# Optimization experiments

Hardware: AMD Instinct MI355X
Metric: run time of the kernel (lower is better)

The kernel has to match this reference:

```python
import jax, jax.numpy as jnp
import numpy as np

S, B, E, H, V, L = 128, 64, 512, 1024, 10000, 2


def setup_inputs() -> dict:
    key = jax.random.key(0)
    ks = jax.random.split(key, 10)
    s = 0.02  # weight scale ~ uniform(-k,k) magnitude
    return {
        "inputs": jax.random.randint(ks[0], (S, B), 0, V),
        "hidden": jnp.zeros((L, B, H), jnp.float32),
        "emb": jax.random.normal(ks[1], (V, E), jnp.float32) * 0.1,
        "Wx0": jax.random.normal(ks[2], (3, H, E), jnp.float32) * s,
        "Uh0": jax.random.normal(ks[3], (3, H, H), jnp.float32) * s,
        "b0": jax.random.normal(ks[4], (3, H), jnp.float32) * s,
        "Wx1": jax.random.normal(ks[5], (3, H, H), jnp.float32) * s,
        "Uh1": jax.random.normal(ks[6], (3, H, H), jnp.float32) * s,
        "b1": jax.random.normal(ks[7], (3, H), jnp.float32) * s,
        "Wd": jax.random.normal(ks[8], (V, H), jnp.float32) * 0.1,
        "bd": jnp.zeros((V,), jnp.float32),
    }


def _gru_cell(xp, h, U, b):
    # xp: (3,B,H) precomputed input projections in [r,z,h] order
    r = jax.nn.sigmoid(xp[0] + h @ U[0].T + b[0])
    z = jax.nn.sigmoid(xp[1] + h @ U[1].T + b[1])
    h_tilde = jnp.tanh(xp[2] + (r * h) @ U[2].T + b[2])
    return (1.0 - z) * h + z * h_tilde


def reference(inputs, hidden, emb, Wx0, Uh0, b0, Wx1, Uh1, b1, Wd, bd):
    x_embs = emb[inputs]                                   # [S,B,E]
    # precompute layer-0 input projections across all timesteps
    xa0 = jnp.einsum("sbe,goe->sgbo", x_embs, Wx0)        # [S,3,B,H]

    def step(carry, xa0_t):
        h0, h1 = carry
        h0n = _gru_cell(xa0_t, h0, Uh0, b0)
        xp1 = jnp.einsum("bk,gok->gbo", h0n, Wx1)          # [3,B,H]
        h1n = _gru_cell(xp1, h1, Uh1, b1)
        return (h0n, h1n), h1n

    (h0f, h1f), hs1 = jax.lax.scan(step, (hidden[0], hidden[1]), xa0)
    logits = jnp.einsum("sbh,vh->sbv", hs1, Wd) + bd       # [S,B,V]
    return logits, jnp.stack([h0f, h1f])
```

## Files before the change

### kernel.cpp

```cpp
#include <hip/hip_runtime.h>
#include <hip/hip_bf16.h>

#define SLEN 128
#define BAT 64
#define EDIM 512
#define HDIM 1024
#define VOC 10000
#define VPAD 10112
#define NWG_REC 192
#define TPB_REC 512

typedef short v8s __attribute__((ext_vector_type(8)));
typedef float v4f __attribute__((ext_vector_type(4)));
typedef unsigned short u16;

__device__ __forceinline__ u16 f2bf(float f) {
  unsigned u = __float_as_uint(f);
  u += 0x7fffu + ((u >> 16) & 1u);
  return (u16)(u >> 16);
}
__device__ __forceinline__ float bf2f(u16 b) {
  return __uint_as_float(((unsigned)b) << 16);
}
__device__ __forceinline__ float sigm(float x) { return 1.f / (1.f + __expf(-x)); }
__device__ __forceinline__ float tanh_f(float x) { return 1.f - 2.f / (1.f + __expf(2.f * x)); }

__device__ __forceinline__ void st_f32(float* p, float v) {
  __hip_atomic_store(p, v, __ATOMIC_RELAXED, __HIP_MEMORY_SCOPE_AGENT);
}
__device__ __forceinline__ float ld_f32(const float* p) {
  return __hip_atomic_load(p, __ATOMIC_RELAXED, __HIP_MEMORY_SCOPE_AGENT);
}
__device__ __forceinline__ float ld_bf16(const unsigned* base, int elem) {
  unsigned pr = __hip_atomic_load(base + (elem >> 1), __ATOMIC_RELAXED, __HIP_MEMORY_SCOPE_AGENT);
  return bf2f((u16)((elem & 1) ? (pr >> 16) : (pr & 0xffffu)));
}
__device__ __forceinline__ void st_bf16_pair(unsigned* base, int elem, u16 val, int l) {
  unsigned p = (unsigned)__shfl_xor((int)val, 1);
  if ((l & 1) == 0)
    __hip_atomic_store(base + (elem >> 1), (unsigned)val | (p << 16),
                       __ATOMIC_RELAXED, __HIP_MEMORY_SCOPE_AGENT);
}

__device__ __forceinline__ void gbar_full(int* bar, int ph, int wg, int t) {
  asm volatile("s_waitcnt vmcnt(0) lgkmcnt(0)" ::: "memory");
  __syncthreads();
  if (t == 0)
    __hip_atomic_store(&bar[wg], ph, __ATOMIC_RELAXED, __HIP_MEMORY_SCOPE_AGENT);
  if (t < 64) {
    for (;;) {
      int v0 = __hip_atomic_load(&bar[t],       __ATOMIC_RELAXED, __HIP_MEMORY_SCOPE_AGENT);
      int v1 = __hip_atomic_load(&bar[64 + t],  __ATOMIC_RELAXED, __HIP_MEMORY_SCOPE_AGENT);
      int v2 = __hip_atomic_load(&bar[128 + t], __ATOMIC_RELAXED, __HIP_MEMORY_SCOPE_AGENT);
      if (__all((v0 >= ph) & (v1 >= ph) & (v2 >= ph))) break;
      __builtin_amdgcn_s_sleep(1);
    }
  }
  __syncthreads();
}

__device__ __forceinline__ void gbar_inv(int* bar, int ph, int wg, int t,
                                         int xcc, bool lead) {
  asm volatile("s_waitcnt vmcnt(0) lgkmcnt(0)" ::: "memory");
  __syncthreads();
  if (t == 0)
    __hip_atomic_store(&bar[wg], ph, __ATOMIC_RELAXED, __HIP_MEMORY_SCOPE_AGENT);
  if (lead) {
    if (t < 64) {
      for (;;) {
        int v0 = __hip_atomic_load(&bar[t],       __ATOMIC_RELAXED, __HIP_MEMORY_SCOPE_AGENT);
        int v1 = __hip_atomic_load(&bar[64 + t],  __ATOMIC_RELAXED, __HIP_MEMORY_SCOPE_AGENT);
        int v2 = __hip_atomic_load(&bar[128 + t], __ATOMIC_RELAXED, __HIP_MEMORY_SCOPE_AGENT);
        if (__all((v0 >= ph) & (v1 >= ph) & (v2 >= ph))) break;
        __builtin_amdgcn_s_sleep(1);
      }
      if (t == 0) {
        asm volatile("buffer_inv sc1" ::: "memory");
        asm volatile("s_waitcnt vmcnt(0)" ::: "memory");
        __hip_atomic_store(&bar[256 + xcc], ph, __ATOMIC_RELAXED, __HIP_MEMORY_SCOPE_AGENT);
      }
    }
  } else {
    if (t < 64) {
      while (__hip_atomic_load(&bar[256 + xcc], __ATOMIC_RELAXED, __HIP_MEMORY_SCOPE_AGENT) < ph)
        __builtin_amdgcn_s_sleep(1);
    }
  }
  if (t < 64) {
    asm volatile("buffer_inv" ::: "memory");
    asm volatile("s_waitcnt vmcnt(0)" ::: "memory");
  }
  __syncthreads();
}

__device__ __forceinline__ v4f gemm_staged(const char* Asrc, char* stage,
                                           const char* bb, int swz,
                                           int t, int rg, int lr, int lk2) {
  const char* gp = Asrc + (t >> 3) * 2048 + (t & 7) * 16;
  char* wp = stage + (t >> 3) * 128 + (((t & 7) * 16) ^ (((t >> 3) & 7) << 4));
  const char* rp = stage + (rg * 16 + lr) * 128;
  v4f acc{0.f, 0.f, 0.f, 0.f};
  v8s sreg[3];
  asm volatile("global_load_dwordx4 %0, %1, off" : "=v"(sreg[0]) : "v"(gp));
  asm volatile("global_load_dwordx4 %0, %1, off offset:128" : "=v"(sreg[1]) : "v"(gp));
  asm volatile("global_load_dwordx4 %0, %1, off offset:256" : "=v"(sreg[2]) : "v"(gp));
  asm volatile("s_waitcnt vmcnt(2)" ::: "memory");
  __builtin_amdgcn_sched_barrier(0);
  *(v8s*)wp = sreg[0];
  __syncthreads();
#pragma unroll
  for (int c = 0; c < 16; ++c) {
    if (c < 13)
      asm volatile("global_load_dwordx4 %0, %1, off offset:%2"
                   : "=v"(sreg[c % 3]) : "v"(gp), "i"((c + 3) * 128));
    if (c < 15) {
      if (c < 13)       asm volatile("s_waitcnt vmcnt(2)" ::: "memory");
      else if (c == 13) asm volatile("s_waitcnt vmcnt(1)" ::: "memory");
      else              asm volatile("s_waitcnt vmcnt(0)" ::: "memory");
      __builtin_amdgcn_sched_barrier(0);
      *(v8s*)(wp + ((c + 1) & 1) * 8192) = sreg[(c + 1) % 3];
    }
    const char* buf = rp + (c & 1) * 8192;
#pragma unroll
    for (int ls = 0; ls < 2; ++ls) {
      v8s a = *(const v8s*)(buf + ((ls * 64 + lk2) ^ swz));
      v8s b = *(const v8s*)(bb + (((c * 2 + ls) * 64 + lk2) ^ swz));
      acc = __builtin_amdgcn_mfma_f32_16x16x32_bf16(a, b, acc, 0, 0, 0);
    }
    __syncthreads();
  }
  return acc;
}

__global__ void __launch_bounds__(TPB_REC, 2) k_recur(
    const u16* __restrict__ Uh0b, const u16* __restrict__ Wx1b, const u16* __restrict__ Uh1b,
    const float* __restrict__ b0, const float* __restrict__ b1,
    const u16* __restrict__ xa0,
    float* __restrict__ h0f, u16* __restrict__ h0b,
    float* __restrict__ h1f, u16* __restrict__ h1b,
    u16* __restrict__ a2, float* __restrict__ z0,
    u16* __restrict__ a5, float* __restrict__ z1,
    u16* __restrict__ xp1,
    u16* __restrict__ hs1,
    float* __restrict__ outh,
    int* __restrict__ bar) {
  extern __shared__ char smem[];
  const int wg = blockIdx.x;
  const int t = threadIdx.x;
  const int w = t >> 6;
  const int l = t & 63;
  const int lr = l & 15;
  const int lk2 = (l >> 4) * 16;
  const int rg = w >> 1, cg = w & 1;
  const int rbase = rg * 16 + ((l >> 4) << 2);
  const int swz = (lr & 7) << 4;
  char* stage = smem + 131072;

  unsigned* a2u  = (unsigned*)a2;
  unsigned* a5u  = (unsigned*)a5;
  unsigned* h0bu = (unsigned*)h0b;
  unsigned* h1bu = (unsigned*)h1b;
  unsigned* xpu  = (unsigned*)xp1;
  unsigned* hs1u = (unsigned*)hs1;

  {
    const u16* w1src; int w1row0;
    if (wg < 64)       { w1src = Uh0b; w1row0 = wg * 32; }
    else if (wg < 160) { w1src = Wx1b; w1row0 = (wg - 64) * 32; }
    else               { w1src = Uh1b; w1row0 = 2048 + (wg - 160) * 32; }
    for (int i = t; i < 4096; i += TPB_REC) {
      int c = i >> 7, j = i & 127;
      v8s v = *(const v8s*)(w1src + (size_t)(w1row0 + c) * HDIM + j * 8);
      *(v8s*)(smem + c * 2048 + ((j * 16) ^ ((c & 7) << 4))) = v;
    }
    if (wg < 96) {
      const u16* w2src; int w2row0;
      if (wg < 32) { w2src = Uh0b; w2row0 = 2048 + wg * 32; }
      else         { w2src = Uh1b; w2row0 = (wg - 32) * 32; }
      for (int i = t; i < 4096; i += TPB_REC) {
        int c = i >> 7, j = i & 127;
        v8s v = *(const v8s*)(w2src + (size_t)(w2row0 + c) * HDIM + j * 8);
        *(v8s*)(smem + 65536 + c * 2048 + ((j * 16) ^ ((c & 7) << 4))) = v;
      }
    }
    __syncthreads();
  }

  int xcc;
  asm volatile("s_getreg_b32 %0, hwreg(HW_REG_XCC_ID)" : "=s"(xcc));
  xcc &= 7;
  if (t == 0)
    (void)__hip_atomic_fetch_min(&bar[320 + xcc], wg, __ATOMIC_RELAXED, __HIP_MEMORY_SCOPE_AGENT);
  gbar_full(bar, 1, wg, t);
  const bool lead =
      (__hip_atomic_load(&bar[320 + xcc], __ATOMIC_RELAXED, __HIP_MEMORY_SCOPE_AGENT) == wg);

  const char* bb1 = smem + (cg * 16 + lr) * 2048;
  const char* bb2 = smem + 65536 + (cg * 16 + lr) * 2048;

  for (int T = 0; T <= SLEN + 1; ++T) {
    if (wg < 64) {
      if (T < SLEN) {
        const int cglob = wg * 32 + cg * 16 + lr;
        const int g = cglob >> 10;
        const int o = cglob & 1023;
        const float bias = b0[g * HDIM + o];
        float xv[4], hv[4];
#pragma unroll
        for (int r = 0; r < 4; ++r) {
          int b = rbase + r;
          xv[r] = bf2f(xa0[((T * 3 + g) * BAT + b) * HDIM + o]);
          if (g == 0) hv[r] = ld_f32(&h0f[b * HDIM + o]);
        }
        v4f acc = gemm_staged((const char*)h0b, stage, bb1, swz, t, rg, lr, lk2);
#pragma unroll
        for (int r = 0; r < 4; ++r) {
          int b = rbase + r;
          float s = sigm(acc[r] + xv[r] + bias);
          if (g == 0) st_bf16_pair(a2u, b * HDIM + o, f2bf(s * hv[r]), l);
          else        st_f32(&z0[b * HDIM + o], s);
        }
      }
    } else if (wg < 160) {
      if (T >= 1 && T <= SLEN) {
        const int n = (wg - 64) * 32 + cg * 16 + lr;
        v4f acc = gemm_staged((const char*)h0b, stage, bb1, swz, t, rg, lr, lk2);
        unsigned* xp = xpu + ((((T - 1) & 1) * (BAT * 3 * HDIM)) >> 1);
#pragma unroll
        for (int r = 0; r < 4; ++r)
          st_bf16_pair(xp, (rbase + r) * 3072 + n, f2bf(acc[r]), l);
      }
    } else {
      if (T >= 2) {
        const int t5 = T - 2;
        const int o = (wg - 160) * 32 + cg * 16 + lr;
        const unsigned* xp = xpu + (((t5 & 1) * (BAT * 3 * HDIM)) >> 1);
        const float bias = b1[2 * HDIM + o];
        float pv[4], zv[4], hv[4];
#pragma unroll
        for (int r = 0; r < 4; ++r) {
          int b = rbase + r;
          pv[r] = ld_bf16(xp, b * 3072 + 2048 + o);
          zv[r] = ld_f32(&z1[b * HDIM + o]);
          hv[r] = ld_f32(&h1f[b * HDIM + o]);
        }
        v4f acc = gemm_staged((const char*)a5, stage, bb1, swz, t, rg, lr, lk2);
#pragma unroll
        for (int r = 0; r < 4; ++r) {
          int b = rbase + r;
          float ht = tanh_f(pv[r] + acc[r] + bias);
          float hn = (1.f - zv[r]) * hv[r] + zv[r] * ht;
          u16 hb = f2bf(hn);
          st_f32(&h1f[b * HDIM + o], hn);
          st_bf16_pair(h1bu, b * HDIM + o, hb, l);
          st_bf16_pair(hs1u, (int)(((size_t)t5 * BAT + b) * HDIM + o), hb, l);
          if (t5 == SLEN - 1) st_f32(&outh[(size_t)BAT * HDIM + b * HDIM + o], hn);
        }
      }
    }
    gbar_inv(bar, 2 * T + 2, wg, t, xcc, lead);
    if (wg < 32) {
      if (T < SLEN) {
        const int o = wg * 32 + cg * 16 + lr;
        const float bias = b0[2 * HDIM + o];
        float xv[4], zv[4], hv[4];
#pragma unroll
        for (int r = 0; r < 4; ++r) {
          int b = rbase + r;
          xv[r] = bf2f(xa0[((T * 3 + 2) * BAT + b) * HDIM + o]);
          zv[r] = ld_f32(&z0[b * HDIM + o]);
          hv[r] = ld_f32(&h0f[b * HDIM + o]);
        }
        v4f acc = gemm_staged((const char*)a2, stage, bb2, swz, t, rg, lr, lk2);
#pragma unroll
        for (int r = 0; r < 4; ++r) {
          int b = rbase + r;
          float ht = tanh_f(xv[r] + acc[r] + bias);
          float hn = (1.f - zv[r]) * hv[r] + zv[r] * ht;
          st_f32(&h0f[b * HDIM + o], hn);
          st_bf16_pair(h0bu, b * HDIM + o, f2bf(hn), l);
          if (T == SLEN - 1) st_f32(&outh[b * HDIM + o], hn);
        }
      }
    } else if (wg < 96) {
      if (T >= 1 && T <= SLEN) {
        const int t4 = T - 1;
        const int cglob = (wg - 32) * 32 + cg * 16 + lr;
        const int g = cglob >> 10;
        const int o = cglob & 1023;
        const unsigned* xp = xpu + (((t4 & 1) * (BAT * 3 * HDIM)) >> 1);
        const float bias = b1[g * HDIM + o];
        float pv[4], hv[4];
#pragma unroll
        for (int r = 0; r < 4; ++r) {
          int b = rbase + r;
          pv[r] = ld_bf16(xp, b * 3072 + g * HDIM + o);
          if (g == 0) hv[r] = ld_f32(&h1f[b * HDIM + o]);
        }
        v4f acc = gemm_staged((const char*)h1b, stage, bb2, swz, t, rg, lr, lk2);
#pragma unroll
        for (int r = 0; r < 4; ++r) {
          int b = rbase + r;
          float s = sigm(acc[r] + pv[r] + bias);
          if (g == 0) st_bf16_pair(a5u, b * HDIM + o, f2bf(s * hv[r]), l);
          else        st_f32(&z1[b * HDIM + o], s);
        }
      }
    }
    gbar_inv(bar, 2 * T + 3, wg, t, xcc, lead);
  }
}

template <int MODE>
__global__ void __launch_bounds__(256) k_gemm(
    const u16* __restrict__ A, const u16* __restrict__ Bw,
    const int* __restrict__ gidx, const float* __restrict__ bias,
    void* __restrict__ Out) {
  constexpr int K = MODE ? 1024 : 512;
  constexpr int NB_N = MODE ? (VPAD / 128) : (3072 / 128);

  __shared__ u16 sA[128 * 64];
  __shared__ u16 sB[128 * 64];

  const int nwg = gridDim.x;
  const int cpx = nwg >> 3;
  const int bid = blockIdx.x;
  const int swz = (bid & 7) * cpx + (bid >> 3);
  const int bm = swz / NB_N, bn = swz % NB_N;
  const int m0 = bm * 128, n0 = bn * 128;

  const int t = threadIdx.x;
  const int w = t >> 6, l = t & 63;
  const int lr = l & 15, lk = (l >> 4) * 8;
  const int wm = (w >> 1) * 64, wn = (w & 1) * 64;
  const int kc = (t & 7) * 8;

  int arowg[4];
#pragma unroll
  for (int i = 0; i < 4; ++i) {
    int row = m0 + i * 32 + (t >> 3);
    arowg[i] = (MODE == 0) ? gidx[row] : row;
  }
  int brow[4];
#pragma unroll
  for (int i = 0; i < 4; ++i) brow[i] = n0 + i * 32 + (t >> 3);

  v4f acc[4][4];
#pragma unroll
  for (int mi = 0; mi < 4; ++mi)
#pragma unroll
    for (int ni = 0; ni < 4; ++ni) acc[mi][ni] = v4f{0.f, 0.f, 0.f, 0.f};

  for (int k0 = 0; k0 < K; k0 += 64) {
    __syncthreads();
#pragma unroll
    for (int i = 0; i < 4; ++i) {
      const u16* src = A + (size_t)arowg[i] * K + k0 + kc;
      __builtin_amdgcn_global_load_lds((const __attribute__((address_space(1))) void*)src,
                                       (__attribute__((address_space(3))) void*)(sA + i * 2048 + w * 512),
                                       16, 0, 0);
    }
#pragma unroll
    for (int i = 0; i < 4; ++i) {
      const u16* src = Bw + (size_t)brow[i] * K + k0 + kc;
      __builtin_amdgcn_global_load_lds((const __attribute__((address_space(1))) void*)src,
                                       (__attribute__((address_space(3))) void*)(sB + i * 2048 + w * 512),
                                       16, 0, 0);
    }
    asm volatile("s_waitcnt vmcnt(0)" ::: "memory");
    __syncthreads();
#pragma unroll
    for (int ks = 0; ks < 2; ++ks) {
      v8s af[4], bfr[4];
#pragma unroll
      for (int mi = 0; mi < 4; ++mi) af[mi] = *(const v8s*)&sA[(wm + mi * 16 + lr) * 64 + ks * 32 + lk];
#pragma unroll
      for (int ni = 0; ni < 4; ++ni) bfr[ni] = *(const v8s*)&sB[(wn + ni * 16 + lr) * 64 + ks * 32 + lk];
#pragma unroll
      for (int mi = 0; mi < 4; ++mi)
#pragma unroll
        for (int ni = 0; ni < 4; ++ni)
          acc[mi][ni] = __builtin_amdgcn_mfma_f32_16x16x32_bf16(af[mi], bfr[ni], acc[mi][ni], 0, 0, 0);
    }
  }

#pragma unroll
  for (int mi = 0; mi < 4; ++mi)
#pragma unroll
    for (int ni = 0; ni < 4; ++ni)
#pragma unroll
      for (int r = 0; r < 4; ++r) {
        int grow = m0 + wm + mi * 16 + ((l >> 4) << 2) + r;
        int gcol = n0 + wn + ni * 16 + lr;
        float v = acc[mi][ni][r];
        if (MODE == 0) {
          int s = grow >> 6, b = grow & 63;
          int g = gcol >> 10, o = gcol & 1023;
          ((u16*)Out)[(((size_t)s * 3 + g) * BAT + b) * HDIM + o] = f2bf(v);
        } else {
          if (gcol < VOC) ((float*)Out)[(size_t)grow * VOC + gcol] = v + bias[gcol];
        }
      }
}

__global__ void k_cvt(const float* __restrict__ src, u16* __restrict__ dst, int n, int nsrc) {
  int i = (blockIdx.x * 256 + threadIdx.x) * 4;
  if (i >= n) return;
#pragma unroll
  for (int j = 0; j < 4; ++j) {
    int idx = i + j;
    if (idx < n) dst[idx] = (idx < nsrc) ? f2bf(src[idx]) : (u16)0;
  }
}

__global__ void k_init(const float* __restrict__ hidden,
                       float* h0f, u16* h0b, float* h1f, u16* h1b, int* bar) {
  int i = blockIdx.x * 256 + threadIdx.x;
  if (i < BAT * HDIM) {
    float v0 = hidden[i];
    float v1 = hidden[BAT * HDIM + i];
    h0f[i] = v0; h0b[i] = f2bf(v0);
    h1f[i] = v1; h1b[i] = f2bf(v1);
  }
  if (i < 512) bar[i] = (i >= 320 && i < 328) ? 0x7fffffff : 0;
}

extern "C" void kernel_launch(void* const* d_in, const int* in_sizes, int n_in,
                              void* d_out, int out_size, void* d_ws, size_t ws_size,
                              hipStream_t stream) {
  const int*   inp = (const int*)d_in[0];
  const float* hid = (const float*)d_in[1];
  const float* emb = (const float*)d_in[2];
  const float* Wx0 = (const float*)d_in[3];
  const float* Uh0 = (const float*)d_in[4];
  const float* b0  = (const float*)d_in[5];
  const float* Wx1 = (const float*)d_in[6];
  const float* Uh1 = (const float*)d_in[7];
  const float* b1  = (const float*)d_in[8];
  const float* Wd  = (const float*)d_in[9];
  const float* bd  = (const float*)d_in[10];

  char* ws = (char*)d_ws;
  size_t off = 0;
  auto alloc = [&](size_t bytes) {
    void* p = ws + off;
    off = (off + bytes + 255) & ~(size_t)255;
    return p;
  };
  u16* emb_b = (u16*)alloc(sizeof(u16) * (size_t)VOC * EDIM);
  u16* Wx0_b = (u16*)alloc(sizeof(u16) * 3 * HDIM * EDIM);
  u16* Uh0_b = (u16*)alloc(sizeof(u16) * 3 * HDIM * HDIM);
  u16* Wx1_b = (u16*)alloc(sizeof(u16) * 3 * HDIM * HDIM);
  u16* Uh1_b = (u16*)alloc(sizeof(u16) * 3 * HDIM * HDIM);
  u16* Wd_b  = (u16*)alloc(sizeof(u16) * (size_t)VPAD * HDIM);
  u16* xa0_b = (u16*)alloc(sizeof(u16) * (size_t)SLEN * 3 * BAT * HDIM);
  u16* hs1_b = (u16*)alloc(sizeof(u16) * (size_t)SLEN * BAT * HDIM);
  u16* xp1   = (u16*)alloc(sizeof(u16) * 2 * BAT * 3 * HDIM);
  float* h0f = (float*)alloc(sizeof(float) * BAT * HDIM);
  float* h1f = (float*)alloc(sizeof(float) * BAT * HDIM);
  u16* h0b   = (u16*)alloc(sizeof(u16) * BAT * HDIM);
  u16* h1b   = (u16*)alloc(sizeof(u16) * BAT * HDIM);
  u16* a2    = (u16*)alloc(sizeof(u16) * BAT * HDIM);
  u16* a5    = (u16*)alloc(sizeof(u16) * BAT * HDIM);
  float* z0  = (float*)alloc(sizeof(float) * BAT * HDIM);
  float* z1  = (float*)alloc(sizeof(float) * BAT * HDIM);
  int* bar   = (int*)alloc(sizeof(int) * 512);

  float* logits = (float*)d_out;
  float* outh = logits + (size_t)SLEN * BAT * VOC;

  auto cvt = [&](const float* s, u16* d, int n, int nsrc) {
    k_cvt<<<dim3((n / 4 + 255) / 256), dim3(256), 0, stream>>>(s, d, n, nsrc);
  };
  cvt(emb, emb_b, VOC * EDIM, VOC * EDIM);
  cvt(Wx0, Wx0_b, 3 * HDIM * EDIM, 3 * HDIM * EDIM);
  cvt(Uh0, Uh0_b, 3 * HDIM * HDIM, 3 * HDIM * HDIM);
  cvt(Wx1, Wx1_b, 3 * HDIM * HDIM, 3 * HDIM * HDIM);
  cvt(Uh1, Uh1_b, 3 * HDIM * HDIM, 3 * HDIM * HDIM);
  cvt(Wd, Wd_b, VPAD * HDIM, VOC * HDIM);
  k_init<<<dim3(256), dim3(256), 0, stream>>>(hid, h0f, h0b, h1f, h1b, bar);

  k_gemm<0><<<dim3(64 * 24), dim3(256), 0, stream>>>(emb_b, Wx0_b, inp, (const float*)nullptr, (void*)xa0_b);

  (void)hipFuncSetAttribute(reinterpret_cast<const void*>(k_recur),
                            hipFuncAttributeMaxDynamicSharedMemorySize, 147456);
  k_recur<<<dim3(NWG_REC), dim3(TPB_REC), 147456, stream>>>(
      Uh0_b, Wx1_b, Uh1_b, b0, b1, xa0_b,
      h0f, h0b, h1f, h1b, a2, z0, a5, z1, xp1, hs1_b, outh, bar);

  k_gemm<1><<<dim3(64 * 79), dim3(256), 0, stream>>>(hs1_b, Wd_b, (const int*)nullptr, bd, d_out);
}
```

Before: 2.476 ms.

## Load recurrent GEMM activations directly from global into registers, dropping LDS staging

Replaces the LDS-staged A-operand path in the recurrent kernel's per-step GEMM with direct global loads into registers, keeping eight loads in flight. It accumulates into two alternating MFMA accumulators. This removes the per-chunk __syncthreads and LDS write/read round-trips, and shrinks dynamic shared memory by 16 KB. Each wave now fetches its own A rows from global/L2, so the two column-group waves load the same data twice, and more registers are used.

```diff
diff --git a/kernel.cpp b/kernel.cpp
--- a/kernel.cpp
+++ b/kernel.cpp
@@ -93,43 +93,26 @@
   __syncthreads();
 }
 
-__device__ __forceinline__ v4f gemm_staged(const char* Asrc, char* stage,
-                                           const char* bb, int swz,
-                                           int t, int rg, int lr, int lk2) {
-  const char* gp = Asrc + (t >> 3) * 2048 + (t & 7) * 16;
-  char* wp = stage + (t >> 3) * 128 + (((t & 7) * 16) ^ (((t >> 3) & 7) << 4));
-  const char* rp = stage + (rg * 16 + lr) * 128;
-  v4f acc{0.f, 0.f, 0.f, 0.f};
-  v8s sreg[3];
-  asm volatile("global_load_dwordx4 %0, %1, off" : "=v"(sreg[0]) : "v"(gp));
-  asm volatile("global_load_dwordx4 %0, %1, off offset:128" : "=v"(sreg[1]) : "v"(gp));
-  asm volatile("global_load_dwordx4 %0, %1, off offset:256" : "=v"(sreg[2]) : "v"(gp));
-  asm volatile("s_waitcnt vmcnt(2)" ::: "memory");
-  __builtin_amdgcn_sched_barrier(0);
-  *(v8s*)wp = sreg[0];
-  __syncthreads();
-#pragma unroll
-  for (int c = 0; c < 16; ++c) {
-    if (c < 13)
+__device__ __forceinline__ v4f gemm_direct(const char* apl, const char* bcl,
+                                           int swz, int lk2) {
+  v8s a[8];
+  v4f acc0{0.f, 0.f, 0.f, 0.f}, acc1{0.f, 0.f, 0.f, 0.f};
+#pragma unroll
+  for (int j = 0; j < 8; ++j)
+    asm volatile("global_load_dwordx4 %0, %1, off offset:%2"
+                 : "=v"(a[j]) : "v"(apl), "i"(j * 64));
+#pragma unroll
+  for (int ks = 0; ks < 32; ++ks) {
+    asm volatile("s_waitcnt vmcnt(%0)" :: "i"((ks < 24) ? 7 : (31 - ks)));
+    __builtin_amdgcn_sched_barrier(0x3F6);
+    v8s b = *(const v8s*)(bcl + ((ks * 64 + lk2) ^ swz));
+    if (ks & 1) acc1 = __builtin_amdgcn_mfma_f32_16x16x32_bf16(a[ks & 7], b, acc1, 0, 0, 0);
+    else        acc0 = __builtin_amdgcn_mfma_f32_16x16x32_bf16(a[ks & 7], b, acc0, 0, 0, 0);
+    if (ks < 24)
       asm volatile("global_load_dwordx4 %0, %1, off offset:%2"
-                   : "=v"(sreg[c % 3]) : "v"(gp), "i"((c + 3) * 128));
-    if (c < 15) {
-      if (c < 13)       asm volatile("s_waitcnt vmcnt(2)" ::: "memory");
-      else if (c == 13) asm volatile("s_waitcnt vmcnt(1)" ::: "memory");
-      else              asm volatile("s_waitcnt vmcnt(0)" ::: "memory");
-      __builtin_amdgcn_sched_barrier(0);
-      *(v8s*)(wp + ((c + 1) & 1) * 8192) = sreg[(c + 1) % 3];
-    }
-    const char* buf = rp + (c & 1) * 8192;
-#pragma unroll
-    for (int ls = 0; ls < 2; ++ls) {
-      v8s a = *(const v8s*)(buf + ((ls * 64 + lk2) ^ swz));
-      v8s b = *(const v8s*)(bb + (((c * 2 + ls) * 64 + lk2) ^ swz));
-      acc = __builtin_amdgcn_mfma_f32_16x16x32_bf16(a, b, acc, 0, 0, 0);
-    }
-    __syncthreads();
-  }
-  return acc;
+                   : "=v"(a[ks & 7]) : "v"(apl), "i"((ks + 8) * 64));
+  }
+  return acc0 + acc1;
 }
 
 __global__ void __launch_bounds__(TPB_REC, 2) k_recur(
@@ -154,7 +137,6 @@
   const int rg = w >> 1, cg = w & 1;
   const int rbase = rg * 16 + ((l >> 4) << 2);
   const int swz = (lr & 7) << 4;
-  char* stage = smem + 131072;
 
   unsigned* a2u  = (unsigned*)a2;
   unsigned* a5u  = (unsigned*)a5;
@@ -197,6 +179,7 @@
 
   const char* bb1 = smem + (cg * 16 + lr) * 2048;
   const char* bb2 = smem + 65536 + (cg * 16 + lr) * 2048;
+  const int arow = (rg * 16 + lr) * 2048 + lk2;
 
   for (int T = 0; T <= SLEN + 1; ++T) {
     if (wg < 64) {
@@ -212,7 +195,7 @@
           xv[r] = bf2f(xa0[((T * 3 + g) * BAT + b) * HDIM + o]);
           if (g == 0) hv[r] = ld_f32(&h0f[b * HDIM + o]);
         }
-        v4f acc = gemm_staged((const char*)h0b, stage, bb1, swz, t, rg, lr, lk2);
+        v4f acc = gemm_direct((const char*)h0b + arow, bb1, swz, lk2);
 #pragma unroll
         for (int r = 0; r < 4; ++r) {
           int b = rbase + r;
@@ -224,7 +207,7 @@
     } else if (wg < 160) {
       if (T >= 1 && T <= SLEN) {
         const int n = (wg - 64) * 32 + cg * 16 + lr;
-        v4f acc = gemm_staged((const char*)h0b, stage, bb1, swz, t, rg, lr, lk2);
+        v4f acc = gemm_direct((const char*)h0b + arow, bb1, swz, lk2);
         unsigned* xp = xpu + ((((T - 1) & 1) * (BAT * 3 * HDIM)) >> 1);
 #pragma unroll
         for (int r = 0; r < 4; ++r)
@@ -244,7 +227,7 @@
           zv[r] = ld_f32(&z1[b * HDIM + o]);
           hv[r] = ld_f32(&h1f[b * HDIM + o]);
         }
-        v4f acc = gemm_staged((const char*)a5, stage, bb1, swz, t, rg, lr, lk2);
+        v4f acc = gemm_direct((const char*)a5 + arow, bb1, swz, lk2);
 #pragma unroll
         for (int r = 0; r < 4; ++r) {
           int b = rbase + r;
@@ -271,7 +254,7 @@
           zv[r] = ld_f32(&z0[b * HDIM + o]);
           hv[r] = ld_f32(&h0f[b * HDIM + o]);
         }
-        v4f acc = gemm_staged((const char*)a2, stage, bb2, swz, t, rg, lr, lk2);
+        v4f acc = gemm_direct((const char*)a2 + arow, bb2, swz, lk2);
 #pragma unroll
         for (int r = 0; r < 4; ++r) {
           int b = rbase + r;
@@ -297,7 +280,7 @@
           pv[r] = ld_bf16(xp, b * 3072 + g * HDIM + o);
           if (g == 0) hv[r] = ld_f32(&h1f[b * HDIM + o]);
         }
-        v4f acc = gemm_staged((const char*)h1b, stage, bb2, swz, t, rg, lr, lk2);
+        v4f acc = gemm_direct((const char*)h1b + arow, bb2, swz, lk2);
 #pragma unroll
         for (int r = 0; r < 4; ++r) {
           int b = rbase + r;
@@ -483,8 +466,8 @@
   k_gemm<0><<<dim3(64 * 24), dim3(256), 0, stream>>>(emb_b, Wx0_b, inp, (const float*)nullptr, (void*)xa0_b);
 
   (void)hipFuncSetAttribute(reinterpret_cast<const void*>(k_recur),
-                            hipFuncAttributeMaxDynamicSharedMemorySize, 147456);
-  k_recur<<<dim3(NWG_REC), dim3(TPB_REC), 147456, stream>>>(
+                            hipFuncAttributeMaxDynamicSharedMemorySize, 131072);
+  k_recur<<<dim3(NWG_REC), dim3(TPB_REC), 131072, stream>>>(
       Uh0_b, Wx1_b, Uh1_b, b0, b1, xa0_b,
       h0f, h0b, h1f, h1b, a2, z0, a5, z1, xp1, hs1_b, outh, bar);
 
```

New measurement: 3.881 ms. 56.7% more time.

## Stream A-operand chunks directly into LDS with a triple-buffered pipeline

Applied to the files above, without the earlier changes.

The staged GEMM in the recurrent kernel now uses global_load_lds to copy activation chunks straight from global memory into LDS. This skips the round trip through VGPRs and the explicit ds_write. Staging grows from a double buffer to a triple buffer, with three chunks in flight, so dynamic LDS rises to 155648 bytes. The swizzle moves to the global-address side, and each chunk now takes an extra barrier. The change saves register pressure and write instructions, but the per-chunk synchronisation becomes heavier.

```diff
diff --git a/kernel.cpp b/kernel.cpp
--- a/kernel.cpp
+++ b/kernel.cpp
@@ -96,39 +96,34 @@
 __device__ __forceinline__ v4f gemm_staged(const char* Asrc, char* stage,
                                            const char* bb, int swz,
                                            int t, int rg, int lr, int lk2) {
-  const char* gp = Asrc + (t >> 3) * 2048 + (t & 7) * 16;
-  char* wp = stage + (t >> 3) * 128 + (((t & 7) * 16) ^ (((t >> 3) & 7) << 4));
+  const int w = t >> 6;
+  const int srow = t >> 3;
+  const int scol = ((t & 7) * 16) ^ ((srow & 7) << 4);
+  const char* gp = Asrc + srow * 2048 + scol;
+  char* wbase = stage + w * 1024;
   const char* rp = stage + (rg * 16 + lr) * 128;
   v4f acc{0.f, 0.f, 0.f, 0.f};
-  v8s sreg[3];
-  asm volatile("global_load_dwordx4 %0, %1, off" : "=v"(sreg[0]) : "v"(gp));
-  asm volatile("global_load_dwordx4 %0, %1, off offset:128" : "=v"(sreg[1]) : "v"(gp));
-  asm volatile("global_load_dwordx4 %0, %1, off offset:256" : "=v"(sreg[2]) : "v"(gp));
-  asm volatile("s_waitcnt vmcnt(2)" ::: "memory");
-  __builtin_amdgcn_sched_barrier(0);
-  *(v8s*)wp = sreg[0];
-  __syncthreads();
+#define ISSUE_CH(c, b)                                                          \
+  __builtin_amdgcn_global_load_lds(                                             \
+      (const __attribute__((address_space(1))) void*)(gp + (c) * 128),          \
+      (__attribute__((address_space(3))) void*)(wbase + (b) * 8192), 16, 0, 0)
+  ISSUE_CH(0, 0); ISSUE_CH(1, 1); ISSUE_CH(2, 2);
 #pragma unroll
   for (int c = 0; c < 16; ++c) {
-    if (c < 13)
-      asm volatile("global_load_dwordx4 %0, %1, off offset:%2"
-                   : "=v"(sreg[c % 3]) : "v"(gp), "i"((c + 3) * 128));
-    if (c < 15) {
-      if (c < 13)       asm volatile("s_waitcnt vmcnt(2)" ::: "memory");
-      else if (c == 13) asm volatile("s_waitcnt vmcnt(1)" ::: "memory");
-      else              asm volatile("s_waitcnt vmcnt(0)" ::: "memory");
-      __builtin_amdgcn_sched_barrier(0);
-      *(v8s*)(wp + ((c + 1) & 1) * 8192) = sreg[(c + 1) % 3];
-    }
-    const char* buf = rp + (c & 1) * 8192;
-#pragma unroll
-    for (int ls = 0; ls < 2; ++ls) {
-      v8s a = *(const v8s*)(buf + ((ls * 64 + lk2) ^ swz));
-      v8s b = *(const v8s*)(bb + (((c * 2 + ls) * 64 + lk2) ^ swz));
-      acc = __builtin_amdgcn_mfma_f32_16x16x32_bf16(a, b, acc, 0, 0, 0);
-    }
+    asm volatile("s_waitcnt vmcnt(%0)" :: "i"((c <= 13) ? 2 : (15 - c)) : "memory");
+    __builtin_amdgcn_sched_barrier(0);
     __syncthreads();
-  }
+    const char* buf = rp + (c % 3) * 8192;
+    v8s a0  = *(const v8s*)(buf + ((0 * 64 + lk2) ^ swz));
+    v8s b0v = *(const v8s*)(bb + (((c * 2 + 0) * 64 + lk2) ^ swz));
+    v8s a1  = *(const v8s*)(buf + ((1 * 64 + lk2) ^ swz));
+    v8s b1v = *(const v8s*)(bb + (((c * 2 + 1) * 64 + lk2) ^ swz));
+    acc = __builtin_amdgcn_mfma_f32_16x16x32_bf16(a0, b0v, acc, 0, 0, 0);
+    acc = __builtin_amdgcn_mfma_f32_16x16x32_bf16(a1, b1v, acc, 0, 0, 0);
+    __syncthreads();
+    if (c + 3 < 16) ISSUE_CH(c + 3, c % 3);
+  }
+#undef ISSUE_CH
   return acc;
 }
 
@@ -483,8 +478,8 @@
   k_gemm<0><<<dim3(64 * 24), dim3(256), 0, stream>>>(emb_b, Wx0_b, inp, (const float*)nullptr, (void*)xa0_b);
 
   (void)hipFuncSetAttribute(reinterpret_cast<const void*>(k_recur),
-                            hipFuncAttributeMaxDynamicSharedMemorySize, 147456);
-  k_recur<<<dim3(NWG_REC), dim3(TPB_REC), 147456, stream>>>(
+                            hipFuncAttributeMaxDynamicSharedMemorySize, 155648);
+  k_recur<<<dim3(NWG_REC), dim3(TPB_REC), 155648, stream>>>(
       Uh0_b, Wx1_b, Uh1_b, b0, b1, xa0_b,
       h0f, h0b, h1f, h1b, a2, z0, a5, z1, xp1, hs1_b, outh, bar);
 
```

Measured after the change: 4.031 ms. 1.63x slower.
